# Optimization experiments

Measured on AMD Instinct MI355X. Metric: run time of the kernel, lower is better.

The kernel has to match this reference:

```python
import jax, jax.numpy as jnp
import numpy as np

B_, L_, DM, E, H, R, K = 8, 2048, 512, 64, 64, 4, 3

def setup_inputs() -> dict:
    key = jax.random.key(0)
    ks = jax.random.split(key, 9)
    s = 0.02
    x = jax.random.normal(ks[0], (B_, L_, DM), dtype=jnp.float32)
    W_in = jax.random.normal(ks[1], (DM, 2 * E), dtype=jnp.float32) * s
    conv_w = jax.random.normal(ks[2], (E, K), dtype=jnp.float32) * s   # depthwise kernel per channel
    conv_b = jnp.zeros((E,), dtype=jnp.float32)
    W_x = jax.random.normal(ks[3], (E, R + 2 * H), dtype=jnp.float32) * s
    W_dt = jax.random.normal(ks[4], (R, E), dtype=jnp.float32) * s
    b_dt = jax.random.normal(ks[5], (E,), dtype=jnp.float32) * s
    A_log = jnp.log(jnp.broadcast_to(jnp.arange(1, H + 1, dtype=jnp.float32), (E, H)))
    D = jnp.ones((E,), dtype=jnp.float32)
    W_out = jax.random.normal(ks[6], (E, DM), dtype=jnp.float32) * s
    return {"x": x, "W_in": W_in, "conv_w": conv_w, "conv_b": conv_b,
            "W_x": W_x, "W_dt": W_dt, "b_dt": b_dt, "A_log": A_log, "D": D, "W_out": W_out}

def _causal_dwconv(x, w, b):
    # x: [b, l, E]; w: [E, K]; equivalent to Conv1d(groups=E, padding=K-1)[..., :l]
    xp = jnp.pad(x, ((0, 0), (K - 1, 0), (0, 0)))
    y = b
    for j in range(K):
        y = y + xp[:, j:j + x.shape[1], :] * w[:, j]
    return y

def _mamba(x, W_in, conv_w, conv_b, W_x, W_dt, b_dt, A_log, D, W_out):
    l = x.shape[1]
    xz = x @ W_in                                   # [b, l, 2E]
    xp, res = xz[..., :E], xz[..., E:]
    xp = jax.nn.silu(_causal_dwconv(xp, conv_w, conv_b))
    x_dbl = xp @ W_x                                # [b, l, R+2H]
    dlt, Bm, Cm = x_dbl[..., :R], x_dbl[..., R:R + H], x_dbl[..., R + H:]
    delta = jax.nn.softplus(dlt @ W_dt + b_dt)      # [b, l, E]
    A = -jnp.exp(A_log)                             # [E, H]
    deltaA = jnp.exp(jnp.einsum('bld,dn->bldn', delta, A))
    dBu = jnp.einsum('bld,bln,bld->bldn', delta, Bm, xp)
    state0 = jnp.zeros((x.shape[0], E, H), dtype=x.dtype)
    def step(s, inp):
        dA_t, dBu_t, C_t = inp
        s = dA_t * s + dBu_t                        # [b, E, H]
        y_t = jnp.einsum('bdn,bn->bd', s, C_t)
        return s, y_t
    xs = (jnp.swapaxes(deltaA, 0, 1), jnp.swapaxes(dBu, 0, 1), jnp.swapaxes(Cm, 0, 1))
    _, ys = jax.lax.scan(step, state0, xs)          # [l, b, E]
    y = jnp.swapaxes(ys, 0, 1) + xp * D
    y = y * jax.nn.sigmoid(res)
    return y @ W_out

def reference(x, W_in, conv_w, conv_b, W_x, W_dt, b_dt, A_log, D, W_out):
    return _mamba(x, W_in, conv_w, conv_b, W_x, W_dt, b_dt, A_log, D, W_out)
```

## Files before the change

### kernel.cpp

```cpp
#include <hip/hip_runtime.h>
#include <hip/hip_bf16.h>

#define B_ 8
#define L_ 2048
#define DM 512
#define E_ 64
#define H_ 64
#define R_ 4
#define KC 3
#define BL (B_*L_)
#define NX 132
#define LC 128
#define NCH (L_/LC)

typedef __attribute__((ext_vector_type(8))) short bfrag;
typedef __attribute__((ext_vector_type(4))) float facc;
typedef unsigned int u32;

#define LOG2E 1.4426950408889634f

__device__ __forceinline__ unsigned short f2b(float f) {
  __hip_bfloat16 h = __float2bfloat16(f);
  return *reinterpret_cast<unsigned short*>(&h);
}
__device__ __forceinline__ float b2f16(unsigned short u) {
  return __uint_as_float((unsigned)u << 16);
}
__device__ __forceinline__ bfrag ld_frag(const unsigned short* p) {
  bfrag t;
  __builtin_memcpy(&t, p, 16);
  return t;
}

__global__ __launch_bounds__(64) void k_wfuse(
    const float* __restrict__ Wx, const float* __restrict__ Wdt,
    const float* __restrict__ Win, const float* __restrict__ Wout,
    unsigned short* __restrict__ WFT, unsigned short* __restrict__ WinTk,
    unsigned short* __restrict__ WoutT)
{
  if (blockIdx.x >= 256) {
    const int gid = (blockIdx.x - 256) * 64 + threadIdx.x;
    #pragma unroll
    for (int i = gid; i < E_ * DM; i += 4096) {
      int e = i >> 9, n = i & 511;
      WoutT[n * 64 + e] = f2b(Wout[i]);
    }
    return;
  }
  if (blockIdx.x >= 192) {
    const int gid = (blockIdx.x - 192) * 64 + threadIdx.x;
    const float4* src = (const float4*)Win;
    #pragma unroll
    for (int i = gid; i < DM * 128 / 4; i += 4096) {
      float4 v = src[i];
      ushort4 u;
      u.x = f2b(v.x); u.y = f2b(v.y); u.z = f2b(v.z); u.w = f2b(v.w);
      *(ushort4*)&WinTk[i * 4] = u;
    }
    return;
  }
  const int n = blockIdx.x;
  const int e = threadIdx.x;
  float v;
  if (n < 64) {
    v = 0.f;
    #pragma unroll
    for (int j = 0; j < R_; ++j)
      v = fmaf(Wx[e * NX + j], Wdt[j * 64 + n], v);
  } else if (n < 128) {
    v = Wx[e * NX + R_ + (n - 64)];
  } else {
    v = Wx[e * NX + R_ + 64 + (n - 128)];
  }
  WFT[n * 64 + e] = f2b(v);
}

__global__ __launch_bounds__(256) void k_gemm_in(
    const float* __restrict__ x, const unsigned short* __restrict__ WinTk,
    float* __restrict__ xp_pre, float* __restrict__ resT)
{
  __shared__ unsigned short As[32][72];
  __shared__ unsigned short Bs[128][72];
  const int tid  = threadIdx.x;
  const int m0   = blockIdx.x * 32;
  const int b    = m0 >> 11;
  const int l0   = m0 & 2047;
  const int lane = tid & 63;
  const int wave = tid >> 6;
  const int mt   = wave & 1;
  const int ng   = wave >> 1;
  const int nl   = lane & 15;
  const int g    = lane >> 4;
  const int ar = tid >> 3;
  const int aq = tid & 7;
  const int bn = tid & 127;
  const int kq = tid >> 7;

  facc acc[4];
  #pragma unroll
  for (int j = 0; j < 4; ++j) acc[j] = (facc)(0.f);

  for (int it = 0; it < 8; ++it) {
    const int k0 = it * 64;
    if (it) __syncthreads();
    #pragma unroll
    for (int p = 0; p < 2; ++p) {
      float4 v = *(const float4*)&x[(size_t)(m0 + ar) * DM + k0 + aq * 8 + 4 * p];
      ushort4 u;
      u.x = f2b(v.x); u.y = f2b(v.y); u.z = f2b(v.z); u.w = f2b(v.w);
      *(ushort4*)&As[ar][aq * 8 + 4 * p] = u;
    }
    #pragma unroll
    for (int p = 0; p < 8; ++p) {
      const unsigned short* wp = &WinTk[(size_t)(k0 + kq * 32 + 4 * p) * 128 + bn];
      u32 lo = (u32)wp[0]   | ((u32)wp[128] << 16);
      u32 hi = (u32)wp[256] | ((u32)wp[384] << 16);
      uint2 uu; uu.x = lo; uu.y = hi;
      *(uint2*)&Bs[bn][kq * 32 + 4 * p] = uu;
    }
    __syncthreads();
    #pragma unroll
    for (int ks = 0; ks < 2; ++ks) {
      bfrag af = ld_frag(&As[mt * 16 + nl][ks * 32 + g * 8]);
      #pragma unroll
      for (int nt2 = 0; nt2 < 4; ++nt2) {
        bfrag bfr = ld_frag(&Bs[(ng * 4 + nt2) * 16 + nl][ks * 32 + g * 8]);
        acc[nt2] = __builtin_amdgcn_mfma_f32_16x16x32_bf16(af, bfr, acc[nt2], 0, 0, 0);
      }
    }
  }
  #pragma unroll
  for (int nt2 = 0; nt2 < 4; ++nt2) {
    facc a = acc[nt2];
    int c = (ng * 4 + nt2) * 16 + nl;
    int mrow = mt * 16 + 4 * g;
    if (c < 64) {
      #pragma unroll
      for (int r = 0; r < 4; ++r)
        xp_pre[(size_t)(m0 + mrow + r) * 64 + c] = a[r];
    } else {
      *(float4*)&resT[(size_t)(b * 64 + (c - 64)) * L_ + l0 + mrow] =
          make_float4(a[0], a[1], a[2], a[3]);
    }
  }
}

__global__ __launch_bounds__(256) void k_fused(
    const float* __restrict__ xp_pre,
    const float* __restrict__ conv_w, const float* __restrict__ conv_b,
    const unsigned short* __restrict__ WFT, const float* __restrict__ bdt,
    float* __restrict__ xpT, float* __restrict__ deltaT,
    u32* __restrict__ BCm)
{
  __shared__ float raw[66][65];
  __shared__ unsigned short rawb[64][72];
  __shared__ unsigned short WFb[192][72];
  const int tid = threadIdx.x;
  const int grp = blockIdx.x >> 1;
  const int yh  = blockIdx.x & 1;
  const int t0 = grp * 64;
  const int b  = t0 >> 11;
  const int l0 = t0 & 2047;
  for (int fidx = tid; fidx < 66 * 16; fidx += 256) {
    int r = fidx >> 4, cg = fidx & 15;
    int l = l0 - 2 + r;
    float4 v = make_float4(0.f, 0.f, 0.f, 0.f);
    if (l >= 0) v = *(const float4*)&xp_pre[((size_t)b * L_ + l) * 64 + cg * 4];
    raw[r][cg * 4 + 0] = v.x;
    raw[r][cg * 4 + 1] = v.y;
    raw[r][cg * 4 + 2] = v.z;
    raw[r][cg * 4 + 3] = v.w;
  }
  {
    const int nbase = yh ? 64 : 0;
    const int nrows = yh ? 128 : 64;
    for (int i4 = tid; i4 < nrows * 16; i4 += 256) {
      int n = nbase + (i4 >> 4), jq = i4 & 15;
      *(ushort4*)&WFb[n][jq * 4] = *(const ushort4*)&WFT[n * 64 + jq * 4];
    }
  }
  __syncthreads();
  const int e  = tid & 63;
  const int tl = tid >> 6;
  const float w0 = conv_w[e * KC + 0], w1 = conv_w[e * KC + 1], w2 = conv_w[e * KC + 2];
  const float cb = conv_b[e];
  float cres[16];
  #pragma unroll
  for (int i = 0; i < 16; ++i) {
    int tok = tl * 16 + i;
    float a = cb;
    a = fmaf(raw[tok + 0][e], w0, a);
    a = fmaf(raw[tok + 1][e], w1, a);
    a = fmaf(raw[tok + 2][e], w2, a);
    cres[i] = a / (1.f + __expf(-a));
  }
  #pragma unroll
  for (int i = 0; i < 16; ++i) rawb[tl * 16 + i][e] = f2b(cres[i]);
  if (yh == 0) {
    #pragma unroll
    for (int i = 0; i < 16; i += 4)
      *(float4*)&xpT[(size_t)(b * 64 + e) * L_ + l0 + tl * 16 + i] =
          make_float4(cres[i], cres[i + 1], cres[i + 2], cres[i + 3]);
  }
  __syncthreads();
  const int wave = tid >> 6;
  const int lane = tid & 63;
  const int nl   = lane & 15;
  const int g    = lane >> 4;
  const int mrow = wave * 16 + 4 * g;
  if (yh == 0) {
    facc acc[4];
    #pragma unroll
    for (int j = 0; j < 4; ++j) acc[j] = (facc)(0.f);
    #pragma unroll
    for (int ks = 0; ks < 2; ++ks) {
      bfrag af = ld_frag(&rawb[wave * 16 + nl][ks * 32 + g * 8]);
      #pragma unroll
      for (int nt = 0; nt < 4; ++nt) {
        bfrag bfr = ld_frag(&WFb[nt * 16 + nl][ks * 32 + g * 8]);
        acc[nt] = __builtin_amdgcn_mfma_f32_16x16x32_bf16(af, bfr, acc[nt], 0, 0, 0);
      }
    }
    #pragma unroll
    for (int nt = 0; nt < 4; ++nt) {
      facc a = acc[nt];
      int c = nt * 16 + nl;
      float bias = bdt[c];
      float d0 = a[0] + bias, d1 = a[1] + bias, d2 = a[2] + bias, d3 = a[3] + bias;
      float4 dv;
      dv.x = (d0 > 20.f) ? d0 : log1pf(__expf(d0));
      dv.y = (d1 > 20.f) ? d1 : log1pf(__expf(d1));
      dv.z = (d2 > 20.f) ? d2 : log1pf(__expf(d2));
      dv.w = (d3 > 20.f) ? d3 : log1pf(__expf(d3));
      *(float4*)&deltaT[(size_t)(b * 64 + c) * L_ + l0 + mrow] = dv;
    }
  } else {
    facc acc[8];
    #pragma unroll
    for (int j = 0; j < 8; ++j) acc[j] = (facc)(0.f);
    #pragma unroll
    for (int ks = 0; ks < 2; ++ks) {
      bfrag af = ld_frag(&rawb[wave * 16 + nl][ks * 32 + g * 8]);
      #pragma unroll
      for (int j = 0; j < 8; ++j) {
        bfrag bfr = ld_frag(&WFb[(4 + j) * 16 + nl][ks * 32 + g * 8]);
        acc[j] = __builtin_amdgcn_mfma_f32_16x16x32_bf16(af, bfr, acc[j], 0, 0, 0);
      }
    }
    #pragma unroll
    for (int j = 0; j < 4; ++j) {
      facc aB = acc[j];
      facc aC = acc[4 + j];
      int col = j * 16 + nl;
      #pragma unroll
      for (int r = 0; r < 4; ++r)
        BCm[(size_t)(t0 + mrow + r) * 64 + col] =
            (u32)f2b(aB[r]) | ((u32)f2b(aC[r]) << 16);
    }
  }
}

__global__ __launch_bounds__(256) void k_scan1(
    const float* __restrict__ deltaT, const float* __restrict__ xpT,
    const u32* __restrict__ BCm, const float* __restrict__ A_log,
    float* __restrict__ Ssum, float* __restrict__ Pp)
{
  __shared__ float dwA[4][256];
  const int tid = threadIdx.x;
  const int wv  = tid >> 6;
  const int h   = tid & 63;
  const int id  = blockIdx.x * 4 + wv;
  const int c   = id & (NCH - 1);
  if (c == NCH - 1) return;
  const int e = (id >> 4) & 63;
  const int b = id >> 10;
  const float A2 = -__expf(A_log[e * 64 + h]) * LOG2E;
  const size_t beL = (size_t)(b * 64 + e) * L_;
  const int l0 = c * LC;
  float* dw = dwA[wv];
  {
    float2 dv = *(const float2*)&deltaT[beL + l0 + 2 * h];
    float2 xv = *(const float2*)&xpT[beL + l0 + 2 * h];
    *(float2*)&dw[2 * h] = dv;
    *(float2*)&dw[128 + 2 * h] = make_float2(dv.x * xv.x, dv.y * xv.y);
  }
  const u32* bc = &BCm[(size_t)(b * L_ + l0) * 64 + h];
  float s = 0.f, sd = 0.f;
  #pragma unroll 2
  for (int k16 = 0; k16 < 8; ++k16) {
    #pragma unroll
    for (int kk = 0; kk < 16; ++kk) {
      const int k = k16 * 16 + kk;
      float dlt = dw[k];
      float w   = dw[128 + k];
      u32 u = bc[(size_t)k * 64];
      float Bh = __uint_as_float(u << 16);
      s = fmaf(__builtin_amdgcn_exp2f(dlt * A2), s, w * Bh);
      sd += dlt;
    }
  }
  const size_t idx = (size_t)id * 64 + h;
  Ssum[idx] = s;
  Pp[idx]   = __builtin_amdgcn_exp2f(A2 * sd);
}

__global__ __launch_bounds__(256) void k_scan3(
    const float* __restrict__ deltaT, const float* __restrict__ xpT,
    const float* __restrict__ resT, const u32* __restrict__ BCm,
    const float* __restrict__ A_log, const float* __restrict__ Dp,
    const float* __restrict__ Ssum, const float* __restrict__ Pp,
    unsigned short* __restrict__ ygTh)
{
  __shared__ float tileA[4][16][68];
  __shared__ float bufA[4][512];
  const int tid = threadIdx.x;
  const int wv  = tid >> 6;
  const int h   = tid & 63;
  const int id  = blockIdx.x * 4 + wv;
  const int c   = id & (NCH - 1);
  const int e   = (id >> 4) & 63;
  const int b   = id >> 10;
  const float A2 = -__expf(A_log[e * 64 + h]) * LOG2E;
  const float Dv = Dp[e];
  const size_t beL = (size_t)(b * 64 + e) * L_;
  float (*tile)[68] = tileA[wv];
  float* buf = bufA[wv];
  float s = 0.f;
  const size_t sbase = (size_t)(id & ~(NCH - 1)) * 64 + h;
  for (int cc = 0; cc < c; ++cc)
    s = fmaf(Pp[sbase + (size_t)cc * 64], s, Ssum[sbase + (size_t)cc * 64]);
  const int l0 = c * LC;
  {
    float2 dv = *(const float2*)&deltaT[beL + l0 + 2 * h];
    float2 xv = *(const float2*)&xpT[beL + l0 + 2 * h];
    float2 rv = *(const float2*)&resT[beL + l0 + 2 * h];
    *(float2*)&buf[2 * h]       = dv;
    *(float2*)&buf[128 + 2 * h] = make_float2(dv.x * xv.x, dv.y * xv.y);
    *(float2*)&buf[256 + 2 * h] = xv;
    *(float2*)&buf[384 + 2 * h] = rv;
  }
  const u32* bc = &BCm[(size_t)(b * L_ + l0) * 64 + h];
  const int r = h & 15, q = h >> 4;
  #pragma unroll 2
  for (int k16 = 0; k16 < 8; ++k16) {
    #pragma unroll
    for (int kk = 0; kk < 16; ++kk) {
      const int k = k16 * 16 + kk;
      float dlt = buf[k];
      float w   = buf[128 + k];
      u32 u = bc[(size_t)k * 64];
      s = fmaf(__builtin_amdgcn_exp2f(dlt * A2), s, w * __uint_as_float(u << 16));
      tile[kk][h] = s * __uint_as_float(u & 0xffff0000u);
    }
    float part = 0.f;
    const float4* rp = (const float4*)&tile[r][q * 16];
    #pragma unroll
    for (int jq = 0; jq < 4; ++jq) {
      float4 v = rp[jq];
      part += (v.x + v.y) + (v.z + v.w);
    }
    part += __shfl_xor(part, 16, 64);
    part += __shfl_xor(part, 32, 64);
    if (q == 0) {
      const int lk = k16 * 16 + r;
      float y = fmaf(buf[256 + lk], Dv, part);
      y *= __builtin_amdgcn_rcpf(1.f + __builtin_amdgcn_exp2f(-LOG2E * buf[384 + lk]));
      ygTh[beL + l0 + lk] = f2b(y);
    }
  }
}

__global__ __launch_bounds__(128) void k_gemm_out(
    const unsigned short* __restrict__ ygTh, const unsigned short* __restrict__ WoutT,
    float* __restrict__ out)
{
  __shared__ unsigned short As[64][68];
  __shared__ unsigned short Bs[128][68];
  const int tid  = threadIdx.x;
  const int m0   = (blockIdx.x & 255) * 64;
  const int n0   = (blockIdx.x >> 8) * 128;
  const int b    = m0 >> 11;
  const int l0   = m0 & 2047;
  const int lane = tid & 63;
  const int wave = tid >> 6;
  const int nl   = lane & 15;
  const int g    = lane >> 4;
  #pragma unroll
  for (int p = 0; p < 8; ++p) {
    int fidx = tid + 128 * p;
    int e = fidx >> 4, q = fidx & 15;
    ushort4 v = *(const ushort4*)&ygTh[(size_t)(b * 64 + e) * L_ + l0 + 4 * q];
    As[4 * q + 0][e] = v.x;
    As[4 * q + 1][e] = v.y;
    As[4 * q + 2][e] = v.z;
    As[4 * q + 3][e] = v.w;
  }
  #pragma unroll
  for (int p = 0; p < 16; ++p) {
    int fidx = tid + 128 * p;
    int n = fidx >> 4, jq = fidx & 15;
    *(ushort4*)&Bs[n][4 * jq] = *(const ushort4*)&WoutT[(size_t)(n0 + n) * 64 + 4 * jq];
  }
  __syncthreads();
  facc acc[2][8];
  #pragma unroll
  for (int i = 0; i < 2; ++i)
    #pragma unroll
    for (int j = 0; j < 8; ++j)
      acc[i][j] = (facc)(0.f);
  #pragma unroll
  for (int ks = 0; ks < 2; ++ks) {
    bfrag af0 = ld_frag(&As[wave * 32 + nl][ks * 32 + g * 8]);
    bfrag af1 = ld_frag(&As[wave * 32 + 16 + nl][ks * 32 + g * 8]);
    #pragma unroll
    for (int nt = 0; nt < 8; ++nt) {
      bfrag bfr = ld_frag(&Bs[nt * 16 + nl][ks * 32 + g * 8]);
      acc[0][nt] = __builtin_amdgcn_mfma_f32_16x16x32_bf16(af0, bfr, acc[0][nt], 0, 0, 0);
      acc[1][nt] = __builtin_amdgcn_mfma_f32_16x16x32_bf16(af1, bfr, acc[1][nt], 0, 0, 0);
    }
  }
  #pragma unroll
  for (int mt = 0; mt < 2; ++mt) {
    int mrow = m0 + wave * 32 + mt * 16 + 4 * g;
    #pragma unroll
    for (int nt = 0; nt < 8; ++nt) {
      facc a = acc[mt][nt];
      int c = n0 + nt * 16 + nl;
      #pragma unroll
      for (int r = 0; r < 4; ++r)
        out[(size_t)(mrow + r) * DM + c] = a[r];
    }
  }
}

extern "C" void kernel_launch(void* const* d_in, const int* in_sizes, int n_in,
                              void* d_out, int out_size, void* d_ws, size_t ws_size,
                              hipStream_t stream) {
  const float* x      = (const float*)d_in[0];
  const float* Win    = (const float*)d_in[1];
  const float* conv_w = (const float*)d_in[2];
  const float* conv_b = (const float*)d_in[3];
  const float* Wx     = (const float*)d_in[4];
  const float* Wdt    = (const float*)d_in[5];
  const float* bdt    = (const float*)d_in[6];
  const float* A_log  = (const float*)d_in[7];
  const float* Dp     = (const float*)d_in[8];
  const float* Wout   = (const float*)d_in[9];
  float* out = (float*)d_out;

  float* ws = (float*)d_ws;
  const size_t SZ = (size_t)BL * 64;
  const size_t CH = (size_t)B_ * E_ * NCH * 64;
  float* xp_pre = ws + 0 * SZ;
  float* resT   = ws + 1 * SZ;
  float* xpT    = ws + 2 * SZ;
  float* deltaT = ws + 3 * SZ;
  u32*   BCm    = (u32*)(ws + 4 * SZ);
  float* Ssum   = ws + 6 * SZ;
  float* Pp     = ws + 6 * SZ + 1 * CH;
  unsigned short* WFT = (unsigned short*)(ws + 6 * SZ + 2 * CH);
  unsigned short* base5 = (unsigned short*)(ws + 5 * SZ);
  unsigned short* ygTh  = base5;
  unsigned short* WinTk = base5 + (1u << 20);
  unsigned short* WoutT = WinTk + DM * 128;

  hipLaunchKernelGGL(k_wfuse,    dim3(320),               dim3(64),  0, stream,
                     Wx, Wdt, Win, Wout, WFT, WinTk, WoutT);
  hipLaunchKernelGGL(k_gemm_in,  dim3(BL / 32),           dim3(256), 0, stream,
                     x, WinTk, xp_pre, resT);
  hipLaunchKernelGGL(k_fused,    dim3(BL / 32),           dim3(256), 0, stream,
                     xp_pre, conv_w, conv_b, WFT, bdt, xpT, deltaT, BCm);
  hipLaunchKernelGGL(k_scan1,    dim3(B_ * E_ * NCH / 4), dim3(256), 0, stream,
                     deltaT, xpT, BCm, A_log, Ssum, Pp);
  hipLaunchKernelGGL(k_scan3,    dim3(B_ * E_ * NCH / 4), dim3(256), 0, stream,
                     deltaT, xpT, resT, BCm, A_log, Dp, Ssum, Pp, ygTh);
  hipLaunchKernelGGL(k_gemm_out, dim3(1024),              dim3(128), 0, stream,
                     ygTh, WoutT, out);
}
```

Before: 168.5 us.

## Interleave token pairs in BCm and pack scan inputs for wider loads

BCm is now written so that each 8-byte element holds two consecutive tokens for one channel. Both scan kernels then fetch two timesteps per global load and read the delta and delta*x pairs as a single float4 from LDS. The per-chunk partial state and decay product are merged into one float2 array, and the weight staging buffer in the fused kernel is cut to the rows actually used, lowering LDS use. The intent is fewer load instructions and fewer memory transactions in the latency-bound sequential scans. The risk is a tighter coupling between the producer and consumer layouts.

```diff
diff --git a/kernel.cpp b/kernel.cpp
--- a/kernel.cpp
+++ b/kernel.cpp
@@ -154,7 +154,7 @@
 {
   __shared__ float raw[66][65];
   __shared__ unsigned short rawb[64][72];
-  __shared__ unsigned short WFb[192][72];
+  __shared__ unsigned short WFb[128][72];
   const int tid = threadIdx.x;
   const int grp = blockIdx.x >> 1;
   const int yh  = blockIdx.x & 1;
@@ -175,8 +175,8 @@
     const int nbase = yh ? 64 : 0;
     const int nrows = yh ? 128 : 64;
     for (int i4 = tid; i4 < nrows * 16; i4 += 256) {
-      int n = nbase + (i4 >> 4), jq = i4 & 15;
-      *(ushort4*)&WFb[n][jq * 4] = *(const ushort4*)&WFT[n * 64 + jq * 4];
+      int n = i4 >> 4, jq = i4 & 15;
+      *(ushort4*)&WFb[n][jq * 4] = *(const ushort4*)&WFT[(nbase + n) * 64 + jq * 4];
     }
   }
   __syncthreads();
@@ -243,7 +243,7 @@
       bfrag af = ld_frag(&rawb[wave * 16 + nl][ks * 32 + g * 8]);
       #pragma unroll
       for (int j = 0; j < 8; ++j) {
-        bfrag bfr = ld_frag(&WFb[(4 + j) * 16 + nl][ks * 32 + g * 8]);
+        bfrag bfr = ld_frag(&WFb[j * 16 + nl][ks * 32 + g * 8]);
         acc[j] = __builtin_amdgcn_mfma_f32_16x16x32_bf16(af, bfr, acc[j], 0, 0, 0);
       }
     }
@@ -252,10 +252,14 @@
       facc aB = acc[j];
       facc aC = acc[4 + j];
       int col = j * 16 + nl;
-      #pragma unroll
-      for (int r = 0; r < 4; ++r)
-        BCm[(size_t)(t0 + mrow + r) * 64 + col] =
-            (u32)f2b(aB[r]) | ((u32)f2b(aC[r]) << 16);
+      uint2* dst = (uint2*)BCm + ((size_t)(t0 + mrow) >> 1) * 64 + col;
+      #pragma unroll
+      for (int rr = 0; rr < 2; ++rr) {
+        uint2 v;
+        v.x = (u32)f2b(aB[2 * rr])     | ((u32)f2b(aC[2 * rr])     << 16);
+        v.y = (u32)f2b(aB[2 * rr + 1]) | ((u32)f2b(aC[2 * rr + 1]) << 16);
+        dst[(size_t)rr * 64] = v;
+      }
     }
   }
 }
@@ -263,9 +267,9 @@
 __global__ __launch_bounds__(256) void k_scan1(
     const float* __restrict__ deltaT, const float* __restrict__ xpT,
     const u32* __restrict__ BCm, const float* __restrict__ A_log,
-    float* __restrict__ Ssum, float* __restrict__ Pp)
-{
-  __shared__ float dwA[4][256];
+    float2* __restrict__ SP)
+{
+  __shared__ float4 dwA[4][64];
   const int tid = threadIdx.x;
   const int wv  = tid >> 6;
   const int h   = tid & 63;
@@ -277,42 +281,35 @@
   const float A2 = -__expf(A_log[e * 64 + h]) * LOG2E;
   const size_t beL = (size_t)(b * 64 + e) * L_;
   const int l0 = c * LC;
-  float* dw = dwA[wv];
   {
     float2 dv = *(const float2*)&deltaT[beL + l0 + 2 * h];
     float2 xv = *(const float2*)&xpT[beL + l0 + 2 * h];
-    *(float2*)&dw[2 * h] = dv;
-    *(float2*)&dw[128 + 2 * h] = make_float2(dv.x * xv.x, dv.y * xv.y);
-  }
-  const u32* bc = &BCm[(size_t)(b * L_ + l0) * 64 + h];
+    dwA[wv][h] = make_float4(dv.x, dv.x * xv.x, dv.y, dv.y * xv.y);
+  }
+  const uint2* bcp = (const uint2*)BCm + ((size_t)(b * L_ + l0) >> 1) * 64 + h;
   float s = 0.f, sd = 0.f;
-  #pragma unroll 2
-  for (int k16 = 0; k16 < 8; ++k16) {
-    #pragma unroll
-    for (int kk = 0; kk < 16; ++kk) {
-      const int k = k16 * 16 + kk;
-      float dlt = dw[k];
-      float w   = dw[128 + k];
-      u32 u = bc[(size_t)k * 64];
-      float Bh = __uint_as_float(u << 16);
-      s = fmaf(__builtin_amdgcn_exp2f(dlt * A2), s, w * Bh);
-      sd += dlt;
-    }
-  }
-  const size_t idx = (size_t)id * 64 + h;
-  Ssum[idx] = s;
-  Pp[idx]   = __builtin_amdgcn_exp2f(A2 * sd);
+  #pragma unroll 8
+  for (int p = 0; p < 64; ++p) {
+    float4 dw = dwA[wv][p];
+    uint2 u2 = bcp[(size_t)p * 64];
+    s = fmaf(__builtin_amdgcn_exp2f(dw.x * A2), s, dw.y * __uint_as_float(u2.x << 16));
+    sd += dw.x;
+    s = fmaf(__builtin_amdgcn_exp2f(dw.z * A2), s, dw.w * __uint_as_float(u2.y << 16));
+    sd += dw.z;
+  }
+  SP[(size_t)id * 64 + h] = make_float2(s, __builtin_amdgcn_exp2f(A2 * sd));
 }
 
 __global__ __launch_bounds__(256) void k_scan3(
     const float* __restrict__ deltaT, const float* __restrict__ xpT,
     const float* __restrict__ resT, const u32* __restrict__ BCm,
     const float* __restrict__ A_log, const float* __restrict__ Dp,
-    const float* __restrict__ Ssum, const float* __restrict__ Pp,
+    const float2* __restrict__ SP,
     unsigned short* __restrict__ ygTh)
 {
   __shared__ float tileA[4][16][68];
-  __shared__ float bufA[4][512];
+  __shared__ float4 dwA[4][64];
+  __shared__ float xrA[4][256];
   const int tid = threadIdx.x;
   const int wv  = tid >> 6;
   const int h   = tid & 63;
@@ -324,33 +321,34 @@
   const float Dv = Dp[e];
   const size_t beL = (size_t)(b * 64 + e) * L_;
   float (*tile)[68] = tileA[wv];
-  float* buf = bufA[wv];
+  float* xr = xrA[wv];
   float s = 0.f;
   const size_t sbase = (size_t)(id & ~(NCH - 1)) * 64 + h;
-  for (int cc = 0; cc < c; ++cc)
-    s = fmaf(Pp[sbase + (size_t)cc * 64], s, Ssum[sbase + (size_t)cc * 64]);
+  for (int cc = 0; cc < c; ++cc) {
+    float2 sp = SP[sbase + (size_t)cc * 64];
+    s = fmaf(sp.y, s, sp.x);
+  }
   const int l0 = c * LC;
   {
     float2 dv = *(const float2*)&deltaT[beL + l0 + 2 * h];
     float2 xv = *(const float2*)&xpT[beL + l0 + 2 * h];
     float2 rv = *(const float2*)&resT[beL + l0 + 2 * h];
-    *(float2*)&buf[2 * h]       = dv;
-    *(float2*)&buf[128 + 2 * h] = make_float2(dv.x * xv.x, dv.y * xv.y);
-    *(float2*)&buf[256 + 2 * h] = xv;
-    *(float2*)&buf[384 + 2 * h] = rv;
-  }
-  const u32* bc = &BCm[(size_t)(b * L_ + l0) * 64 + h];
+    dwA[wv][h] = make_float4(dv.x, dv.x * xv.x, dv.y, dv.y * xv.y);
+    *(float2*)&xr[2 * h]       = xv;
+    *(float2*)&xr[128 + 2 * h] = rv;
+  }
+  const uint2* bcp = (const uint2*)BCm + ((size_t)(b * L_ + l0) >> 1) * 64 + h;
   const int r = h & 15, q = h >> 4;
-  #pragma unroll 2
   for (int k16 = 0; k16 < 8; ++k16) {
     #pragma unroll
-    for (int kk = 0; kk < 16; ++kk) {
-      const int k = k16 * 16 + kk;
-      float dlt = buf[k];
-      float w   = buf[128 + k];
-      u32 u = bc[(size_t)k * 64];
-      s = fmaf(__builtin_amdgcn_exp2f(dlt * A2), s, w * __uint_as_float(u << 16));
-      tile[kk][h] = s * __uint_as_float(u & 0xffff0000u);
+    for (int kp = 0; kp < 8; ++kp) {
+      const int p = k16 * 8 + kp;
+      float4 dw = dwA[wv][p];
+      uint2 u2 = bcp[(size_t)p * 64];
+      s = fmaf(__builtin_amdgcn_exp2f(dw.x * A2), s, dw.y * __uint_as_float(u2.x << 16));
+      tile[2 * kp][h] = s * __uint_as_float(u2.x & 0xffff0000u);
+      s = fmaf(__builtin_amdgcn_exp2f(dw.z * A2), s, dw.w * __uint_as_float(u2.y << 16));
+      tile[2 * kp + 1][h] = s * __uint_as_float(u2.y & 0xffff0000u);
     }
     float part = 0.f;
     const float4* rp = (const float4*)&tile[r][q * 16];
@@ -363,8 +361,8 @@
     part += __shfl_xor(part, 32, 64);
     if (q == 0) {
       const int lk = k16 * 16 + r;
-      float y = fmaf(buf[256 + lk], Dv, part);
-      y *= __builtin_amdgcn_rcpf(1.f + __builtin_amdgcn_exp2f(-LOG2E * buf[384 + lk]));
+      float y = fmaf(xr[lk], Dv, part);
+      y *= __builtin_amdgcn_rcpf(1.f + __builtin_amdgcn_exp2f(-LOG2E * xr[128 + lk]));
       ygTh[beL + l0 + lk] = f2b(y);
     }
   }
@@ -456,8 +454,7 @@
   float* xpT    = ws + 2 * SZ;
   float* deltaT = ws + 3 * SZ;
   u32*   BCm    = (u32*)(ws + 4 * SZ);
-  float* Ssum   = ws + 6 * SZ;
-  float* Pp     = ws + 6 * SZ + 1 * CH;
+  float2* SP    = (float2*)(ws + 6 * SZ);
   unsigned short* WFT = (unsigned short*)(ws + 6 * SZ + 2 * CH);
   unsigned short* base5 = (unsigned short*)(ws + 5 * SZ);
   unsigned short* ygTh  = base5;
@@ -471,9 +468,9 @@
   hipLaunchKernelGGL(k_fused,    dim3(BL / 32),           dim3(256), 0, stream,
                      xp_pre, conv_w, conv_b, WFT, bdt, xpT, deltaT, BCm);
   hipLaunchKernelGGL(k_scan1,    dim3(B_ * E_ * NCH / 4), dim3(256), 0, stream,
-                     deltaT, xpT, BCm, A_log, Ssum, Pp);
+                     deltaT, xpT, BCm, A_log, SP);
   hipLaunchKernelGGL(k_scan3,    dim3(B_ * E_ * NCH / 4), dim3(256), 0, stream,
-                     deltaT, xpT, resT, BCm, A_log, Dp, Ssum, Pp, ygTh);
+                     deltaT, xpT, resT, BCm, A_log, Dp, SP, ygTh);
   hipLaunchKernelGGL(k_gemm_out, dim3(1024),              dim3(128), 0, stream,
                      ygTh, WoutT, out);
 }
```

Result: slower. 173.2 us (+2.8%).

## Fuse two-pass chunked scan into one block-per-channel kernel with LDS carries

Applied to the files above, without the earlier changes.

Merges the chunk-summary scan kernel and the output scan kernel into one kernel where a 512-thread block handles a whole (batch, channel) sequence. Each wave computes chunk summaries for two chunks, shares them through LDS, then rescans with the combined prefix. This removes one launch and the global round trip for the chunk carries and prefix. In exchange it uses large dynamic LDS (about 74 KB), runs fewer but larger blocks (512), and has a serial prefix loop per wave. It also shrinks the k_fused weight tile in shared memory by rebasing its row index.

```diff
diff --git a/kernel.cpp b/kernel.cpp
--- a/kernel.cpp
+++ b/kernel.cpp
@@ -154,7 +154,7 @@
 {
   __shared__ float raw[66][65];
   __shared__ unsigned short rawb[64][72];
-  __shared__ unsigned short WFb[192][72];
+  __shared__ unsigned short WFb[128][72];
   const int tid = threadIdx.x;
   const int grp = blockIdx.x >> 1;
   const int yh  = blockIdx.x & 1;
@@ -175,8 +175,8 @@
     const int nbase = yh ? 64 : 0;
     const int nrows = yh ? 128 : 64;
     for (int i4 = tid; i4 < nrows * 16; i4 += 256) {
-      int n = nbase + (i4 >> 4), jq = i4 & 15;
-      *(ushort4*)&WFb[n][jq * 4] = *(const ushort4*)&WFT[n * 64 + jq * 4];
+      int n = i4 >> 4, jq = i4 & 15;
+      *(ushort4*)&WFb[n][jq * 4] = *(const ushort4*)&WFT[(nbase + n) * 64 + jq * 4];
     }
   }
   __syncthreads();
@@ -243,7 +243,7 @@
       bfrag af = ld_frag(&rawb[wave * 16 + nl][ks * 32 + g * 8]);
       #pragma unroll
       for (int j = 0; j < 8; ++j) {
-        bfrag bfr = ld_frag(&WFb[(4 + j) * 16 + nl][ks * 32 + g * 8]);
+        bfrag bfr = ld_frag(&WFb[j * 16 + nl][ks * 32 + g * 8]);
         acc[j] = __builtin_amdgcn_mfma_f32_16x16x32_bf16(af, bfr, acc[j], 0, 0, 0);
       }
     }
@@ -260,112 +260,91 @@
   }
 }
 
-__global__ __launch_bounds__(256) void k_scan1(
+__global__ __launch_bounds__(512) void k_scan(
     const float* __restrict__ deltaT, const float* __restrict__ xpT,
-    const u32* __restrict__ BCm, const float* __restrict__ A_log,
-    float* __restrict__ Ssum, float* __restrict__ Pp)
+    const float* __restrict__ resT, const u32* __restrict__ BCm,
+    const float* __restrict__ A_log, const float* __restrict__ Dp,
+    unsigned short* __restrict__ ygTh)
 {
-  __shared__ float dwA[4][256];
+  extern __shared__ float lds[];
   const int tid = threadIdx.x;
   const int wv  = tid >> 6;
   const int h   = tid & 63;
-  const int id  = blockIdx.x * 4 + wv;
-  const int c   = id & (NCH - 1);
-  if (c == NCH - 1) return;
-  const int e = (id >> 4) & 63;
-  const int b = id >> 10;
-  const float A2 = -__expf(A_log[e * 64 + h]) * LOG2E;
-  const size_t beL = (size_t)(b * 64 + e) * L_;
-  const int l0 = c * LC;
-  float* dw = dwA[wv];
-  {
-    float2 dv = *(const float2*)&deltaT[beL + l0 + 2 * h];
-    float2 xv = *(const float2*)&xpT[beL + l0 + 2 * h];
-    *(float2*)&dw[2 * h] = dv;
-    *(float2*)&dw[128 + 2 * h] = make_float2(dv.x * xv.x, dv.y * xv.y);
-  }
-  const u32* bc = &BCm[(size_t)(b * L_ + l0) * 64 + h];
-  float s = 0.f, sd = 0.f;
-  #pragma unroll 2
-  for (int k16 = 0; k16 < 8; ++k16) {
-    #pragma unroll
-    for (int kk = 0; kk < 16; ++kk) {
-      const int k = k16 * 16 + kk;
-      float dlt = dw[k];
-      float w   = dw[128 + k];
-      u32 u = bc[(size_t)k * 64];
-      float Bh = __uint_as_float(u << 16);
-      s = fmaf(__builtin_amdgcn_exp2f(dlt * A2), s, w * Bh);
-      sd += dlt;
-    }
-  }
-  const size_t idx = (size_t)id * 64 + h;
-  Ssum[idx] = s;
-  Pp[idx]   = __builtin_amdgcn_exp2f(A2 * sd);
-}
-
-__global__ __launch_bounds__(256) void k_scan3(
-    const float* __restrict__ deltaT, const float* __restrict__ xpT,
-    const float* __restrict__ resT, const u32* __restrict__ BCm,
-    const float* __restrict__ A_log, const float* __restrict__ Dp,
-    const float* __restrict__ Ssum, const float* __restrict__ Pp,
-    unsigned short* __restrict__ ygTh)
-{
-  __shared__ float tileA[4][16][68];
-  __shared__ float bufA[4][512];
-  const int tid = threadIdx.x;
-  const int wv  = tid >> 6;
-  const int h   = tid & 63;
-  const int id  = blockIdx.x * 4 + wv;
-  const int c   = id & (NCH - 1);
-  const int e   = (id >> 4) & 63;
-  const int b   = id >> 10;
+  const int e   = blockIdx.x & 63;
+  const int b   = blockIdx.x >> 6;
   const float A2 = -__expf(A_log[e * 64 + h]) * LOG2E;
   const float Dv = Dp[e];
   const size_t beL = (size_t)(b * 64 + e) * L_;
-  float (*tile)[68] = tileA[wv];
-  float* buf = bufA[wv];
-  float s = 0.f;
-  const size_t sbase = (size_t)(id & ~(NCH - 1)) * 64 + h;
-  for (int cc = 0; cc < c; ++cc)
-    s = fmaf(Pp[sbase + (size_t)cc * 64], s, Ssum[sbase + (size_t)cc * 64]);
-  const int l0 = c * LC;
+  float* dw   = lds + wv * 512;
+  float* xr   = lds + 4096 + wv * 512;
+  float* sS   = lds + 8192;
+  float* sP   = lds + 9216;
+  float* tile = lds + 10240 + wv * 1088;
+  const int l00 = wv * 256;
   {
-    float2 dv = *(const float2*)&deltaT[beL + l0 + 2 * h];
-    float2 xv = *(const float2*)&xpT[beL + l0 + 2 * h];
-    float2 rv = *(const float2*)&resT[beL + l0 + 2 * h];
-    *(float2*)&buf[2 * h]       = dv;
-    *(float2*)&buf[128 + 2 * h] = make_float2(dv.x * xv.x, dv.y * xv.y);
-    *(float2*)&buf[256 + 2 * h] = xv;
-    *(float2*)&buf[384 + 2 * h] = rv;
-  }
-  const u32* bc = &BCm[(size_t)(b * L_ + l0) * 64 + h];
+    float4 dv = *(const float4*)&deltaT[beL + l00 + 4 * h];
+    float4 xv = *(const float4*)&xpT  [beL + l00 + 4 * h];
+    float4 rv = *(const float4*)&resT [beL + l00 + 4 * h];
+    dw[8 * h + 0] = dv.x; dw[8 * h + 1] = dv.x * xv.x;
+    dw[8 * h + 2] = dv.y; dw[8 * h + 3] = dv.y * xv.y;
+    dw[8 * h + 4] = dv.z; dw[8 * h + 5] = dv.z * xv.z;
+    dw[8 * h + 6] = dv.w; dw[8 * h + 7] = dv.w * xv.w;
+    *(float4*)&xr[4 * h]       = xv;
+    *(float4*)&xr[256 + 4 * h] = rv;
+  }
+  __builtin_amdgcn_wave_barrier();
+  #pragma unroll
+  for (int cc = 0; cc < 2; ++cc) {
+    const int c = 2 * wv + cc;
+    const u32* bc = &BCm[(size_t)(b * L_ + c * LC) * 64 + h];
+    const float* dwc = dw + cc * 256;
+    float s = 0.f, sd = 0.f;
+    #pragma unroll 4
+    for (int k = 0; k < 128; ++k) {
+      float d = dwc[2 * k], w = dwc[2 * k + 1];
+      u32 u = bc[(size_t)k * 64];
+      s = fmaf(__builtin_amdgcn_exp2f(d * A2), s, w * __uint_as_float(u << 16));
+      sd += d;
+    }
+    sS[c * 64 + h] = s;
+    sP[c * 64 + h] = __builtin_amdgcn_exp2f(A2 * sd);
+  }
+  __syncthreads();
   const int r = h & 15, q = h >> 4;
-  #pragma unroll 2
-  for (int k16 = 0; k16 < 8; ++k16) {
-    #pragma unroll
-    for (int kk = 0; kk < 16; ++kk) {
-      const int k = k16 * 16 + kk;
-      float dlt = buf[k];
-      float w   = buf[128 + k];
-      u32 u = bc[(size_t)k * 64];
-      s = fmaf(__builtin_amdgcn_exp2f(dlt * A2), s, w * __uint_as_float(u << 16));
-      tile[kk][h] = s * __uint_as_float(u & 0xffff0000u);
-    }
-    float part = 0.f;
-    const float4* rp = (const float4*)&tile[r][q * 16];
-    #pragma unroll
-    for (int jq = 0; jq < 4; ++jq) {
-      float4 v = rp[jq];
-      part += (v.x + v.y) + (v.z + v.w);
-    }
-    part += __shfl_xor(part, 16, 64);
-    part += __shfl_xor(part, 32, 64);
-    if (q == 0) {
-      const int lk = k16 * 16 + r;
-      float y = fmaf(buf[256 + lk], Dv, part);
-      y *= __builtin_amdgcn_rcpf(1.f + __builtin_amdgcn_exp2f(-LOG2E * buf[384 + lk]));
-      ygTh[beL + l0 + lk] = f2b(y);
+  #pragma unroll
+  for (int cc = 0; cc < 2; ++cc) {
+    const int c = 2 * wv + cc;
+    float s = 0.f;
+    for (int j = 0; j < c; ++j)
+      s = fmaf(sP[j * 64 + h], s, sS[j * 64 + h]);
+    const u32* bc = &BCm[(size_t)(b * L_ + c * LC) * 64 + h];
+    const float* dwc = dw + cc * 256;
+    const int lb = cc * 128;
+    for (int k16 = 0; k16 < 8; ++k16) {
+      #pragma unroll
+      for (int kk = 0; kk < 16; ++kk) {
+        const int k = k16 * 16 + kk;
+        float d = dwc[2 * k], w = dwc[2 * k + 1];
+        u32 u = bc[(size_t)k * 64];
+        s = fmaf(__builtin_amdgcn_exp2f(d * A2), s, w * __uint_as_float(u << 16));
+        tile[kk * 68 + h] = s * __uint_as_float(u & 0xffff0000u);
+      }
+      float part = 0.f;
+      const float4* rp = (const float4*)&tile[r * 68 + q * 16];
+      #pragma unroll
+      for (int jq = 0; jq < 4; ++jq) {
+        float4 v = rp[jq];
+        part += (v.x + v.y) + (v.z + v.w);
+      }
+      part += __shfl_xor(part, 16, 64);
+      part += __shfl_xor(part, 32, 64);
+      if (q == 0) {
+        const int lk = k16 * 16 + r;
+        float y = fmaf(xr[lb + lk], Dv, part);
+        y *= __builtin_amdgcn_rcpf(1.f + __builtin_amdgcn_exp2f(-LOG2E * xr[256 + lb + lk]));
+        ygTh[beL + c * LC + lk] = f2b(y);
+      }
+      __builtin_amdgcn_wave_barrier();
     }
   }
 }
@@ -456,24 +435,20 @@
   float* xpT    = ws + 2 * SZ;
   float* deltaT = ws + 3 * SZ;
   u32*   BCm    = (u32*)(ws + 4 * SZ);
-  float* Ssum   = ws + 6 * SZ;
-  float* Pp     = ws + 6 * SZ + 1 * CH;
   unsigned short* WFT = (unsigned short*)(ws + 6 * SZ + 2 * CH);
   unsigned short* base5 = (unsigned short*)(ws + 5 * SZ);
   unsigned short* ygTh  = base5;
   unsigned short* WinTk = base5 + (1u << 20);
   unsigned short* WoutT = WinTk + DM * 128;
 
-  hipLaunchKernelGGL(k_wfuse,    dim3(320),               dim3(64),  0, stream,
+  hipLaunchKernelGGL(k_wfuse,    dim3(320),      dim3(64),  0, stream,
                      Wx, Wdt, Win, Wout, WFT, WinTk, WoutT);
-  hipLaunchKernelGGL(k_gemm_in,  dim3(BL / 32),           dim3(256), 0, stream,
+  hipLaunchKernelGGL(k_gemm_in,  dim3(BL / 32),  dim3(256), 0, stream,
                      x, WinTk, xp_pre, resT);
-  hipLaunchKernelGGL(k_fused,    dim3(BL / 32),           dim3(256), 0, stream,
+  hipLaunchKernelGGL(k_fused,    dim3(BL / 32),  dim3(256), 0, stream,
                      xp_pre, conv_w, conv_b, WFT, bdt, xpT, deltaT, BCm);
-  hipLaunchKernelGGL(k_scan1,    dim3(B_ * E_ * NCH / 4), dim3(256), 0, stream,
-                     deltaT, xpT, BCm, A_log, Ssum, Pp);
-  hipLaunchKernelGGL(k_scan3,    dim3(B_ * E_ * NCH / 4), dim3(256), 0, stream,
-                     deltaT, xpT, resT, BCm, A_log, Dp, Ssum, Pp, ygTh);
-  hipLaunchKernelGGL(k_gemm_out, dim3(1024),              dim3(128), 0, stream,
+  hipLaunchKernelGGL(k_scan,     dim3(B_ * E_),  dim3(512), 75776, stream,
+                     deltaT, xpT, resT, BCm, A_log, Dp, ygTh);
+  hipLaunchKernelGGL(k_gemm_out, dim3(1024),     dim3(128), 0, stream,
                      ygTh, WoutT, out);
 }
```

Result: slower. 175.3 us (+4.0%).
